# Kernel optimization log

Hardware: AMD Instinct MI355X
Metric: run time of the kernel (lower is better)

The kernel has to match this reference:

```python
import jax, jax.numpy as jnp
import numpy as np

NUM_CLASSES = 80
TOPK = 1000
CONF_THRESH = 0.001
NMS_THRESH = 0.5
CLASS_OFFSET = 4096.0  # > max image coordinate, separates classes for class-aware NMS
M = 300000


def setup_inputs() -> dict:
    key = jax.random.key(0)
    k1, k2, k3, k4 = jax.random.split(key, 4)
    obj_preds = jax.random.normal(k1, (1, M, 1), dtype=jnp.float32)
    cls_preds = jax.random.normal(k2, (1, M, NUM_CLASSES), dtype=jnp.float32)
    # random xyxy boxes inside a 640x640 image
    cxcy = jax.random.uniform(k3, (1, M, 2), dtype=jnp.float32) * 640.0
    wh = jax.random.uniform(k4, (1, M, 2), dtype=jnp.float32) * 128.0 + 1.0
    box_preds = jnp.concatenate([cxcy - wh * 0.5, cxcy + wh * 0.5], axis=-1)
    return {"obj_preds": obj_preds, "cls_preds": cls_preds, "box_preds": box_preds}


def _iou_matrix(boxes):
    # boxes: [K, 4] xyxy -> [K, K] pairwise IoU
    x1, y1, x2, y2 = boxes[:, 0], boxes[:, 1], boxes[:, 2], boxes[:, 3]
    area = jnp.clip(x2 - x1, 0.0) * jnp.clip(y2 - y1, 0.0)
    xx1 = jnp.maximum(x1[:, None], x1[None, :])
    yy1 = jnp.maximum(y1[:, None], y1[None, :])
    xx2 = jnp.minimum(x2[:, None], x2[None, :])
    yy2 = jnp.minimum(y2[:, None], y2[None, :])
    inter = jnp.clip(xx2 - xx1, 0.0) * jnp.clip(yy2 - yy1, 0.0)
    return inter / (area[:, None] + area[None, :] - inter + 1e-9)


def _postprocess(obj_preds, cls_preds, box_preds):
    obj = obj_preds[0]   # [M, 1]
    cls = cls_preds[0]   # [M, C]
    box = box_preds[0]   # [M, 4]

    # sigmoid * sigmoid sqrt-score fusion (no_multi_labels branch)
    fused = jnp.sqrt(jax.nn.sigmoid(obj) * jax.nn.sigmoid(cls))  # [M, C]
    scores = jnp.max(fused, axis=1)     # [M]
    labels = jnp.argmax(fused, axis=1)  # [M]

    # sort-descending + take top-k == lax.top_k
    topk_scores, topk_idxs = jax.lax.top_k(scores, TOPK)
    labels_k = labels[topk_idxs]        # [K]
    boxes_k = box[topk_idxs]            # [K, 4]
    conf_mask = topk_scores > CONF_THRESH

    # multiclass NMS via class-offset trick (boxes of different classes never overlap)
    off = labels_k.astype(boxes_k.dtype)[:, None] * CLASS_OFFSET
    iou = _iou_matrix(boxes_k + off)    # [K, K]

    idx = jnp.arange(TOPK)

    def body(i, keep):
        # suppressed if any earlier, still-kept box overlaps > nms_thresh
        sup = (iou[i] > NMS_THRESH) & keep & (idx < i)
        return keep.at[i].set(keep[i] & ~jnp.any(sup))

    keep = jax.lax.fori_loop(0, TOPK, body, conf_mask)  # [K] bool

    keepf = keep.astype(topk_scores.dtype)
    # fixed-shape output: masked [K, 5] = (score, x1, y1, x2, y2); dropped rows zeroed
    out5 = jnp.concatenate([(topk_scores * keepf)[:, None], boxes_k * keepf[:, None]], axis=1)
    return out5, labels_k, keep


def reference(obj_preds, cls_preds, box_preds):
    return _postprocess(obj_preds, cls_preds, box_preds)
```

## Files before the change

kernel.cpp:

```cpp
#include <hip/hip_runtime.h>
#include <hip/hip_bf16.h>
#include <math.h>

#define NCLS 80
#define TOPK_N 1000
#define CAND_CAP 12288
#define T0 0.91f
#define NB 8192
#define HREP 8
#define RBINS 3072
#define RBIN_LO 0x3F680000u
#define ANCH_INV 524287

#define WS_SCORES   0
#define WS_CAND     1200000
#define WS_TKSCORE  1298304
#define WS_TKANCH   1302304
#define WS_TKLABEL  1306304
#define WS_BOXES    1310304
#define WS_OBX      1326304
#define WS_AREAS    1342304
#define WS_MASK     1346304
#define WS_META     1474304
#define WS_HIST     1474368

typedef unsigned long long u64;

__device__ __forceinline__ float sigmoidf_(float x) {
    return 1.0f / (1.0f + expf(-x));
}

__device__ __forceinline__ u64 make_key2(unsigned s32, int anchor) {
    return ((u64)s32 << 19) | (unsigned)(ANCH_INV - anchor);
}

__device__ __forceinline__ int key_bin(u64 k) {
    unsigned s32 = (unsigned)(k >> 19);
    int d = (int)(s32 - RBIN_LO);
    if (d < 0) d = 0;
    int b = d >> 9;
    if (b > RBINS - 1) b = RBINS - 1;
    return (RBINS - 1) - b;
}

__device__ __forceinline__ void rowmax16(const float4* row, int l,
                                         float& bv, int& bc) {
    float4 v4 = row[l];
    bv = v4.x; bc = l * 4;
    if (v4.y > bv) { bv = v4.y; bc = l * 4 + 1; }
    if (v4.z > bv) { bv = v4.z; bc = l * 4 + 2; }
    if (v4.w > bv) { bv = v4.w; bc = l * 4 + 3; }
    if (l < 4) {
        float4 w4 = row[16 + l];
        int cb = 64 + l * 4;
        if (w4.x > bv) { bv = w4.x; bc = cb; }
        if (w4.y > bv) { bv = w4.y; bc = cb + 1; }
        if (w4.z > bv) { bv = w4.z; bc = cb + 2; }
        if (w4.w > bv) { bv = w4.w; bc = cb + 3; }
    }
    #pragma unroll
    for (int m = 8; m >= 1; m >>= 1) {
        float ov = __shfl_xor(bv, m);
        int oc = __shfl_xor(bc, m);
        if (ov > bv || (ov == bv && oc < bc)) { bv = ov; bc = oc; }
    }
}

__global__ void __launch_bounds__(256)
k1_scores(const float* __restrict__ obj,
          const float* __restrict__ cls,
          u64* __restrict__ cand,
          int* __restrict__ counter, int M) {
    __shared__ int lcount, lbase;
    __shared__ u64 lkeys[64];
    int t = threadIdx.x;
    if (t == 0) lcount = 0;
    __syncthreads();
    int l = t & 15;
    int grp = t >> 4;
    int base = blockIdx.x * 64 + grp * 4;
    if (base < M) {
        const float4* p = (const float4*)(cls + (size_t)base * NCLS);
        float4 a0 = p[l], a1 = p[20 + l], a2 = p[40 + l], a3 = p[60 + l];
        float m0 = fmaxf(fmaxf(a0.x, a0.y), fmaxf(a0.z, a0.w));
        float m1 = fmaxf(fmaxf(a1.x, a1.y), fmaxf(a1.z, a1.w));
        float m2 = fmaxf(fmaxf(a2.x, a2.y), fmaxf(a2.z, a2.w));
        float m3 = fmaxf(fmaxf(a3.x, a3.y), fmaxf(a3.z, a3.w));
        if (l < 4) {
            float4 b0 = p[16 + l], b1 = p[36 + l], b2 = p[56 + l], b3 = p[76 + l];
            m0 = fmaxf(m0, fmaxf(fmaxf(b0.x, b0.y), fmaxf(b0.z, b0.w)));
            m1 = fmaxf(m1, fmaxf(fmaxf(b1.x, b1.y), fmaxf(b1.z, b1.w)));
            m2 = fmaxf(m2, fmaxf(fmaxf(b2.x, b2.y), fmaxf(b2.z, b2.w)));
            m3 = fmaxf(m3, fmaxf(fmaxf(b3.x, b3.y), fmaxf(b3.z, b3.w)));
        }
        #pragma unroll
        for (int s = 8; s >= 1; s >>= 1) {
            m0 = fmaxf(m0, __shfl_xor(m0, s));
            m1 = fmaxf(m1, __shfl_xor(m1, s));
            m2 = fmaxf(m2, __shfl_xor(m2, s));
            m3 = fmaxf(m3, __shfl_xor(m3, s));
        }
        if (l < 4) {
            float mm = (l < 2) ? ((l == 0) ? m0 : m1) : ((l == 2) ? m2 : m3);
            int anchor = base + l;
            float score = sqrtf(sigmoidf_(obj[anchor]) * sigmoidf_(mm));
            if (score > T0) {
                int pos = atomicAdd(&lcount, 1);
                lkeys[pos] = make_key2(__float_as_uint(score), anchor);
            }
        }
    }
    __syncthreads();
    if (t == 0 && lcount > 0) lbase = atomicAdd(counter, lcount);
    __syncthreads();
    int n = lcount;
    if (t < n) {
        int pos = lbase + t;
        if (pos < CAND_CAP) cand[pos] = lkeys[t];
    }
}

__global__ void kf_hist(const float* __restrict__ obj,
                        const float* __restrict__ cls,
                        float* __restrict__ scores,
                        unsigned* __restrict__ hist,
                        const int* __restrict__ meta, int M) {
    int C = meta[2];
    if (C >= TOPK_N && C <= CAND_CAP) return;
    int gw = (blockIdx.x * 256 + threadIdx.x) >> 6;
    int TW = gridDim.x * 4;
    int lane = threadIdx.x & 63;
    int g = lane >> 4, l = lane & 15;
    int rep = blockIdx.x & (HREP - 1);
    for (int a0 = gw * 4; a0 < M; a0 += TW * 4) {
        int anchor = a0 + g;
        if (anchor >= M) continue;
        const float4* row = (const float4*)(cls + (size_t)anchor * NCLS);
        float bv; int bc;
        rowmax16(row, l, bv, bc);
        if (l == 0) {
            float score = sqrtf(sigmoidf_(obj[anchor]) * sigmoidf_(bv));
            scores[anchor] = score;
            atomicAdd(&hist[(size_t)rep * NB + (__float_as_uint(score) >> 17)], 1u);
        }
    }
}

__global__ void k2_scan(const unsigned* __restrict__ hist, int* __restrict__ meta) {
    int C = meta[2];
    if (C >= TOPK_N && C <= CAND_CAP) return;
    int t = threadIdx.x;
    int lane = t & 63, w = t >> 6;
    int base = NB - 1 - t * 8;
    unsigned bins[8]; unsigned s = 0;
    #pragma unroll
    for (int k = 0; k < 8; ++k) {
        unsigned h = 0;
        for (int r = 0; r < HREP; ++r) h += hist[(size_t)r * NB + base - k];
        bins[k] = h; s += h;
    }
    unsigned inc = s;
    for (int d = 1; d < 64; d <<= 1) {
        unsigned pv = __shfl_up(inc, d);
        if (lane >= d) inc += pv;
    }
    __shared__ unsigned wsum[16], woff[16];
    if (lane == 63) wsum[w] = inc;
    __syncthreads();
    if (t == 0) {
        unsigned cum = 0;
        for (int i = 0; i < 16; ++i) { woff[i] = cum; cum += wsum[i]; }
    }
    __syncthreads();
    unsigned excl = woff[w] + inc - s;
    if (excl < TOPK_N && excl + s >= TOPK_N) {
        unsigned cum = excl; int b = base;
        #pragma unroll
        for (int k = 0; k < 8; ++k) {
            unsigned h = bins[k];
            if (cum + h >= TOPK_N) { meta[0] = b; break; }
            cum += h; --b;
        }
    }
}

__global__ void k3_compact(const float* __restrict__ scores,
                           int* __restrict__ meta,
                           u64* __restrict__ cand, int M) {
    int C = meta[2];
    if (C >= TOPK_N && C <= CAND_CAP) return;
    int B = meta[0];
    for (int i = blockIdx.x * 256 + threadIdx.x; i < M; i += gridDim.x * 256) {
        unsigned key = __float_as_uint(scores[i]);
        if ((int)(key >> 17) >= B) {
            int pos = atomicAdd(meta + 3, 1);
            if (pos < CAND_CAP)
                cand[pos] = make_key2(key, i);
        }
    }
}

__global__ void __launch_bounds__(1024)
k4_rank(const u64* __restrict__ cand,
        const int* __restrict__ meta,
        float* __restrict__ tkscore,
        int* __restrict__ tkanchor) {
    __shared__ u64 sorted[CAND_CAP];
    __shared__ unsigned hist[RBINS];
    __shared__ unsigned cnt[RBINS];
    __shared__ unsigned wsum[16], woff[16];
    int t = threadIdx.x;
    int lane = t & 63, w = t >> 6;
    int Cf = meta[2];
    bool fast = (Cf >= TOPK_N && Cf <= CAND_CAP);
    int C = fast ? Cf : meta[3];
    if (C > CAND_CAP) C = CAND_CAP;
    for (int b = t; b < RBINS; b += 1024) { hist[b] = 0; cnt[b] = 0; }
    __syncthreads();
    u64 keys[12]; int nk = 0;
    for (int i = t; i < C; i += 1024) {
        u64 k = cand[i];
        keys[nk++] = k;
        atomicAdd(&hist[key_bin(k)], 1u);
    }
    __syncthreads();
    unsigned h0 = hist[t * 3], h1 = hist[t * 3 + 1], h2 = hist[t * 3 + 2];
    unsigned s = h0 + h1 + h2;
    unsigned inc = s;
    for (int d = 1; d < 64; d <<= 1) {
        unsigned pv = __shfl_up(inc, d);
        if (lane >= d) inc += pv;
    }
    if (lane == 63) wsum[w] = inc;
    __syncthreads();
    if (t == 0) {
        unsigned cum = 0;
        for (int i = 0; i < 16; ++i) { woff[i] = cum; cum += wsum[i]; }
    }
    __syncthreads();
    unsigned base = woff[w] + inc - s;
    hist[t * 3] = base;
    hist[t * 3 + 1] = base + h0;
    hist[t * 3 + 2] = base + h0 + h1;
    __syncthreads();
    nk = 0;
    for (int i = t; i < C; i += 1024) {
        u64 k = keys[nk++];
        int b = key_bin(k);
        unsigned pos = hist[b] + atomicAdd(&cnt[b], 1u);
        sorted[pos] = k;
    }
    __syncthreads();
    for (int p = t; p < C; p += 1024) {
        u64 k = sorted[p];
        int b = key_bin(k);
        unsigned b0 = hist[b], b1 = b0 + cnt[b];
        int r = (int)b0;
        for (unsigned q = b0; q < b1; ++q) r += (sorted[q] > k);
        if (r < TOPK_N) {
            tkscore[r] = __uint_as_float((unsigned)(k >> 19));
            tkanchor[r] = ANCH_INV - (int)(k & 0x7FFFF);
        }
    }
}

__global__ void __launch_bounds__(256)
k4b_gather(const float* __restrict__ cls,
           const float4* __restrict__ box,
           const int* __restrict__ tkanchor,
           int* __restrict__ tklabel,
           float4* __restrict__ boxes_k,
           float4* __restrict__ obx,
           float* __restrict__ areas) {
    int grp = threadIdx.x >> 4, l = threadIdx.x & 15;
    int r = blockIdx.x * 16 + grp;
    if (r >= TOPK_N) return;
    int anchor = tkanchor[r];
    const float4* row = (const float4*)(cls + (size_t)anchor * NCLS);
    float bv; int bc;
    rowmax16(row, l, bv, bc);
    if (l == 0) {
        tklabel[r] = bc;
        float4 b = box[anchor];
        boxes_k[r] = b;
        float off = (float)bc * 4096.0f;
        float4 ob = make_float4(b.x + off, b.y + off, b.z + off, b.w + off);
        obx[r] = ob;
        areas[r] = fmaxf(ob.z - ob.x, 0.0f) * fmaxf(ob.w - ob.y, 0.0f);
    }
}

__global__ void k5_iou(const float4* __restrict__ obx,
                       const float* __restrict__ areas,
                       u64* __restrict__ mask) {
    int i = blockIdx.x * 4 + (threadIdx.x >> 6);
    int lane = threadIdx.x & 63;
    if (i >= TOPK_N) return;
    float4 bi = obx[i];
    float ai = areas[i];
    for (int w = 0; w < 16; ++w) {
        int c = w * 64 + lane;
        bool bit = false;
        if (c < i) {
            float4 bc = obx[c];
            float xx1 = fmaxf(bi.x, bc.x), yy1 = fmaxf(bi.y, bc.y);
            float xx2 = fminf(bi.z, bc.z), yy2 = fminf(bi.w, bc.w);
            float inter = fmaxf(xx2 - xx1, 0.0f) * fmaxf(yy2 - yy1, 0.0f);
            float iou = inter / (ai + areas[c] - inter + 1e-9f);
            bit = iou > 0.5f;
        }
        u64 bal = __ballot(bit);
        if (lane == 0) mask[(size_t)i * 16 + w] = bal;
    }
}

__global__ void __launch_bounds__(1024)
k6_nms(const float* __restrict__ tkscore,
       const u64* __restrict__ mask,
       const int* __restrict__ tklabel,
       const float4* __restrict__ boxes_k,
       float* __restrict__ out) {
    __shared__ u64 kept_s[16], dec_s[16];
    int t = threadIdx.x, w = t >> 6, lane = t & 63;
    bool active = t < TOPK_N;
    u64 sup[16];
    float sc = 0.0f;
    if (active) {
        #pragma unroll
        for (int q = 0; q < 16; ++q) sup[q] = mask[(size_t)t * 16 + q];
        sc = tkscore[t];
    } else {
        #pragma unroll
        for (int q = 0; q < 16; ++q) sup[q] = 0ULL;
    }
    bool conf = active && (sc > 0.001f);
    bool mydec = !conf;
    bool mykept = false;
    u64 db = __ballot(mydec), kb = __ballot(mykept);
    if (lane == 0) { dec_s[w] = db; kept_s[w] = kb; }
    __syncthreads();
    for (int round = 0; round < TOPK_N; ++round) {
        if (!mydec) {
            u64 pend = 0;
            #pragma unroll
            for (int q = 0; q < 16; ++q) pend |= sup[q] & ~dec_s[q];
            if (pend == 0ULL) {
                u64 kk = 0;
                #pragma unroll
                for (int q = 0; q < 16; ++q) kk |= sup[q] & kept_s[q];
                mydec = true; mykept = (kk == 0ULL);
            }
        }
        __syncthreads();
        db = __ballot(mydec); kb = __ballot(mykept);
        if (lane == 0) { dec_s[w] = db; kept_s[w] = kb; }
        __syncthreads();
        u64 a = ~0ULL;
        #pragma unroll
        for (int q = 0; q < 16; ++q) a &= dec_s[q];
        if (a == ~0ULL) break;
    }
    if (active) {
        float k = mykept ? 1.0f : 0.0f;
        float4 b = boxes_k[t];
        out[t * 5 + 0] = sc * k;
        out[t * 5 + 1] = b.x * k;
        out[t * 5 + 2] = b.y * k;
        out[t * 5 + 3] = b.z * k;
        out[t * 5 + 4] = b.w * k;
        out[5 * TOPK_N + t] = (float)tklabel[t];
        out[6 * TOPK_N + t] = k;
    }
}

extern "C" void kernel_launch(void* const* d_in, const int* in_sizes, int n_in,
                              void* d_out, int out_size, void* d_ws, size_t ws_size,
                              hipStream_t stream) {
    const float* obj = (const float*)d_in[0];
    const float* cls = (const float*)d_in[1];
    const float* box = (const float*)d_in[2];
    float* out = (float*)d_out;
    char* ws = (char*)d_ws;
    int M = in_sizes[0];

    float*    scores  = (float*)(ws + WS_SCORES);
    u64*      cand    = (u64*)(ws + WS_CAND);
    float*    tkscore = (float*)(ws + WS_TKSCORE);
    int*      tkanch  = (int*)(ws + WS_TKANCH);
    int*      tklabel = (int*)(ws + WS_TKLABEL);
    float4*   boxes_k = (float4*)(ws + WS_BOXES);
    float4*   obx     = (float4*)(ws + WS_OBX);
    float*    areas   = (float*)(ws + WS_AREAS);
    u64*      mask    = (u64*)(ws + WS_MASK);
    int*      meta    = (int*)(ws + WS_META);
    unsigned* hist    = (unsigned*)(ws + WS_HIST);

    hipMemsetAsync(ws + WS_META, 0, 64 + (size_t)HREP * NB * 4, stream);

    k1_scores<<<(M + 63) / 64, 256, 0, stream>>>(obj, cls, cand, meta + 2, M);
    kf_hist<<<512, 256, 0, stream>>>(obj, cls, scores, hist, meta, M);
    k2_scan<<<1, 1024, 0, stream>>>(hist, meta);
    k3_compact<<<512, 256, 0, stream>>>(scores, meta, cand, M);
    k4_rank<<<1, 1024, 0, stream>>>(cand, meta, tkscore, tkanch);
    k4b_gather<<<(TOPK_N + 15) / 16, 256, 0, stream>>>(cls, (const float4*)box,
                                                       tkanch, tklabel, boxes_k, obx, areas);
    k5_iou<<<(TOPK_N + 3) / 4, 256, 0, stream>>>(obx, areas, mask);
    k6_nms<<<1, 1024, 0, stream>>>(tkscore, mask, tklabel, boxes_k, out);
}
```

Baseline: 190.4 us.

## Fuse fallback hist/scan/compact into one block and gather into rank kernel

Merges the fallback path's histogram, scan and compaction kernels into a single one-block kernel using a shared-memory histogram, which drops the large histogram memset and two launches. It also folds the top-k gather of labels and boxes into the rank kernel through a shared anchor array, removing another launch. The fallback path now scans all anchors with a single block, which would be very slow if it ran. With the default inputs the fast path is probably taken, so the main effect is fewer launches and a smaller memset.

```diff
diff --git a/kernel.cpp b/kernel.cpp
--- a/kernel.cpp
+++ b/kernel.cpp
@@ -6,8 +6,7 @@
 #define TOPK_N 1000
 #define CAND_CAP 12288
 #define T0 0.91f
-#define NB 8192
-#define HREP 8
+#define NB2 8192
 #define RBINS 3072
 #define RBIN_LO 0x3F680000u
 #define ANCH_INV 524287
@@ -15,14 +14,12 @@
 #define WS_SCORES   0
 #define WS_CAND     1200000
 #define WS_TKSCORE  1298304
-#define WS_TKANCH   1302304
-#define WS_TKLABEL  1306304
-#define WS_BOXES    1310304
-#define WS_OBX      1326304
-#define WS_AREAS    1342304
-#define WS_MASK     1346304
-#define WS_META     1474304
-#define WS_HIST     1474368
+#define WS_TKLABEL  1302304
+#define WS_BOXES    1306304
+#define WS_OBX      1322304
+#define WS_AREAS    1338304
+#define WS_MASK     1342304
+#define WS_META     1470304
 
 typedef unsigned long long u64;
 
@@ -120,51 +117,42 @@
     }
 }
 
-__global__ void kf_hist(const float* __restrict__ obj,
-                        const float* __restrict__ cls,
-                        float* __restrict__ scores,
-                        unsigned* __restrict__ hist,
-                        const int* __restrict__ meta, int M) {
+__global__ void __launch_bounds__(1024)
+kfall(const float* __restrict__ obj,
+      const float* __restrict__ cls,
+      float* __restrict__ scores,
+      int* __restrict__ meta,
+      u64* __restrict__ cand, int M) {
     int C = meta[2];
     if (C >= TOPK_N && C <= CAND_CAP) return;
-    int gw = (blockIdx.x * 256 + threadIdx.x) >> 6;
-    int TW = gridDim.x * 4;
-    int lane = threadIdx.x & 63;
-    int g = lane >> 4, l = lane & 15;
-    int rep = blockIdx.x & (HREP - 1);
-    for (int a0 = gw * 4; a0 < M; a0 += TW * 4) {
-        int anchor = a0 + g;
-        if (anchor >= M) continue;
-        const float4* row = (const float4*)(cls + (size_t)anchor * NCLS);
-        float bv; int bc;
-        rowmax16(row, l, bv, bc);
-        if (l == 0) {
-            float score = sqrtf(sigmoidf_(obj[anchor]) * sigmoidf_(bv));
-            scores[anchor] = score;
-            atomicAdd(&hist[(size_t)rep * NB + (__float_as_uint(score) >> 17)], 1u);
-        }
-    }
-}
-
-__global__ void k2_scan(const unsigned* __restrict__ hist, int* __restrict__ meta) {
-    int C = meta[2];
-    if (C >= TOPK_N && C <= CAND_CAP) return;
+    __shared__ unsigned hist[NB2];
+    __shared__ unsigned wsum[16], woff[16];
+    __shared__ int bbin;
     int t = threadIdx.x;
     int lane = t & 63, w = t >> 6;
-    int base = NB - 1 - t * 8;
+    for (int b = t; b < NB2; b += 1024) hist[b] = 0;
+    __syncthreads();
+    for (int a = t; a < M; a += 1024) {
+        const float4* row = (const float4*)(cls + (size_t)a * NCLS);
+        float m = -1e30f;
+        for (int j = 0; j < 20; ++j) {
+            float4 v = row[j];
+            m = fmaxf(m, fmaxf(fmaxf(v.x, v.y), fmaxf(v.z, v.w)));
+        }
+        float score = sqrtf(sigmoidf_(obj[a]) * sigmoidf_(m));
+        scores[a] = score;
+        atomicAdd(&hist[__float_as_uint(score) >> 17], 1u);
+    }
+    __syncthreads();
+    int base = NB2 - 1 - t * 8;
     unsigned bins[8]; unsigned s = 0;
     #pragma unroll
-    for (int k = 0; k < 8; ++k) {
-        unsigned h = 0;
-        for (int r = 0; r < HREP; ++r) h += hist[(size_t)r * NB + base - k];
-        bins[k] = h; s += h;
-    }
+    for (int k = 0; k < 8; ++k) { bins[k] = hist[base - k]; s += bins[k]; }
     unsigned inc = s;
     for (int d = 1; d < 64; d <<= 1) {
         unsigned pv = __shfl_up(inc, d);
         if (lane >= d) inc += pv;
     }
-    __shared__ unsigned wsum[16], woff[16];
     if (lane == 63) wsum[w] = inc;
     __syncthreads();
     if (t == 0) {
@@ -178,24 +166,17 @@
         #pragma unroll
         for (int k = 0; k < 8; ++k) {
             unsigned h = bins[k];
-            if (cum + h >= TOPK_N) { meta[0] = b; break; }
+            if (cum + h >= TOPK_N) { bbin = b; break; }
             cum += h; --b;
         }
     }
-}
-
-__global__ void k3_compact(const float* __restrict__ scores,
-                           int* __restrict__ meta,
-                           u64* __restrict__ cand, int M) {
-    int C = meta[2];
-    if (C >= TOPK_N && C <= CAND_CAP) return;
-    int B = meta[0];
-    for (int i = blockIdx.x * 256 + threadIdx.x; i < M; i += gridDim.x * 256) {
-        unsigned key = __float_as_uint(scores[i]);
+    __syncthreads();
+    int B = bbin;
+    for (int a = t; a < M; a += 1024) {
+        unsigned key = __float_as_uint(scores[a]);
         if ((int)(key >> 17) >= B) {
             int pos = atomicAdd(meta + 3, 1);
-            if (pos < CAND_CAP)
-                cand[pos] = make_key2(key, i);
+            if (pos < CAND_CAP) cand[pos] = make_key2(key, a);
         }
     }
 }
@@ -203,11 +184,17 @@
 __global__ void __launch_bounds__(1024)
 k4_rank(const u64* __restrict__ cand,
         const int* __restrict__ meta,
+        const float* __restrict__ cls,
+        const float4* __restrict__ box,
         float* __restrict__ tkscore,
-        int* __restrict__ tkanchor) {
+        int* __restrict__ tklabel,
+        float4* __restrict__ boxes_k,
+        float4* __restrict__ obx,
+        float* __restrict__ areas) {
     __shared__ u64 sorted[CAND_CAP];
     __shared__ unsigned hist[RBINS];
     __shared__ unsigned cnt[RBINS];
+    __shared__ int anch_s[TOPK_N];
     __shared__ unsigned wsum[16], woff[16];
     int t = threadIdx.x;
     int lane = t & 63, w = t >> 6;
@@ -259,34 +246,25 @@
         for (unsigned q = b0; q < b1; ++q) r += (sorted[q] > k);
         if (r < TOPK_N) {
             tkscore[r] = __uint_as_float((unsigned)(k >> 19));
-            tkanchor[r] = ANCH_INV - (int)(k & 0x7FFFF);
-        }
-    }
-}
-
-__global__ void __launch_bounds__(256)
-k4b_gather(const float* __restrict__ cls,
-           const float4* __restrict__ box,
-           const int* __restrict__ tkanchor,
-           int* __restrict__ tklabel,
-           float4* __restrict__ boxes_k,
-           float4* __restrict__ obx,
-           float* __restrict__ areas) {
-    int grp = threadIdx.x >> 4, l = threadIdx.x & 15;
-    int r = blockIdx.x * 16 + grp;
-    if (r >= TOPK_N) return;
-    int anchor = tkanchor[r];
-    const float4* row = (const float4*)(cls + (size_t)anchor * NCLS);
-    float bv; int bc;
-    rowmax16(row, l, bv, bc);
-    if (l == 0) {
-        tklabel[r] = bc;
-        float4 b = box[anchor];
-        boxes_k[r] = b;
-        float off = (float)bc * 4096.0f;
-        float4 ob = make_float4(b.x + off, b.y + off, b.z + off, b.w + off);
-        obx[r] = ob;
-        areas[r] = fmaxf(ob.z - ob.x, 0.0f) * fmaxf(ob.w - ob.y, 0.0f);
+            anch_s[r] = ANCH_INV - (int)(k & 0x7FFFF);
+        }
+    }
+    __syncthreads();
+    int grp = t >> 4, l = t & 15;
+    for (int r = grp; r < TOPK_N; r += 64) {
+        int anchor = anch_s[r];
+        const float4* row = (const float4*)(cls + (size_t)anchor * NCLS);
+        float bv; int bc;
+        rowmax16(row, l, bv, bc);
+        if (l == 0) {
+            tklabel[r] = bc;
+            float4 b = box[anchor];
+            boxes_k[r] = b;
+            float off = (float)bc * 4096.0f;
+            float4 ob = make_float4(b.x + off, b.y + off, b.z + off, b.w + off);
+            obx[r] = ob;
+            areas[r] = fmaxf(ob.z - ob.x, 0.0f) * fmaxf(ob.w - ob.y, 0.0f);
+        }
     }
 }
 
@@ -386,24 +364,19 @@
     float*    scores  = (float*)(ws + WS_SCORES);
     u64*      cand    = (u64*)(ws + WS_CAND);
     float*    tkscore = (float*)(ws + WS_TKSCORE);
-    int*      tkanch  = (int*)(ws + WS_TKANCH);
     int*      tklabel = (int*)(ws + WS_TKLABEL);
     float4*   boxes_k = (float4*)(ws + WS_BOXES);
     float4*   obx     = (float4*)(ws + WS_OBX);
     float*    areas   = (float*)(ws + WS_AREAS);
     u64*      mask    = (u64*)(ws + WS_MASK);
     int*      meta    = (int*)(ws + WS_META);
-    unsigned* hist    = (unsigned*)(ws + WS_HIST);
-
-    hipMemsetAsync(ws + WS_META, 0, 64 + (size_t)HREP * NB * 4, stream);
+
+    hipMemsetAsync(ws + WS_META, 0, 64, stream);
 
     k1_scores<<<(M + 63) / 64, 256, 0, stream>>>(obj, cls, cand, meta + 2, M);
-    kf_hist<<<512, 256, 0, stream>>>(obj, cls, scores, hist, meta, M);
-    k2_scan<<<1, 1024, 0, stream>>>(hist, meta);
-    k3_compact<<<512, 256, 0, stream>>>(scores, meta, cand, M);
-    k4_rank<<<1, 1024, 0, stream>>>(cand, meta, tkscore, tkanch);
-    k4b_gather<<<(TOPK_N + 15) / 16, 256, 0, stream>>>(cls, (const float4*)box,
-                                                       tkanch, tklabel, boxes_k, obx, areas);
+    kfall<<<1, 1024, 0, stream>>>(obj, cls, scores, meta, cand, M);
+    k4_rank<<<1, 1024, 0, stream>>>(cand, meta, cls, (const float4*)box,
+                                    tkscore, tklabel, boxes_k, obx, areas);
     k5_iou<<<(TOPK_N + 3) / 4, 256, 0, stream>>>(obx, areas, mask);
     k6_nms<<<1, 1024, 0, stream>>>(tkscore, mask, tklabel, boxes_k, out);
 }
```

Result: slower. 208.9 us (+9.7%).
